# Performance work log

Hardware: AMD Instinct MI355X
Metric: run time of the kernel (lower is better)

## Reference

```python
import jax, jax.numpy as jnp
import numpy as np

C = 64


def setup_inputs() -> dict:
    key = jax.random.key(0)
    ks = jax.random.split(key, 7)
    x = jax.random.normal(ks[0], (8, C, 64, 64), dtype=jnp.float32)
    # 1x1 conv weights stored as [out_c, in_c]; biases [out_c]
    s = 1.0 / np.sqrt(C)
    W1 = jax.random.uniform(ks[1], (C, C), jnp.float32, -s, s)
    b1 = jax.random.uniform(ks[2], (C,), jnp.float32, -s, s)
    W2 = jax.random.uniform(ks[3], (C, C), jnp.float32, -s, s)
    b2 = jax.random.uniform(ks[4], (C,), jnp.float32, -s, s)
    W3 = jax.random.uniform(ks[5], (C, C), jnp.float32, -s, s)
    b3 = jax.random.uniform(ks[6], (C,), jnp.float32, -s, s)
    return {"x": x, "W1": W1, "b1": b1, "W2": W2, "b2": b2, "W3": W3, "b3": b3}


def reference(x, W1, b1, W2, b2, W3, b3):
    gamma = 1.0
    b, c, h, w = x.shape
    xf = x.reshape(b, c, h * w)  # [b, c, n]
    # 1x1 convs == per-pixel channel matmuls
    f = jnp.einsum('oc,bcn->bon', W1, xf) + b1[None, :, None]
    g = jnp.einsum('oc,bcn->bon', W2, xf) + b2[None, :, None]
    k = jnp.einsum('oc,bcn->bon', W3, xf) + b3[None, :, None]
    # scores[b,i,j] = sum_c f[b,c,i] * g[b,c,j]; softmax over j
    scores = jnp.einsum('bci,bcj->bij', f, g)
    attn = jax.nn.softmax(scores, axis=2)
    # out_attn[b,c,i] = sum_j attn[b,i,j] * k[b,c,j]
    out = jnp.einsum('bij,bcj->bci', attn, k).reshape(b, c, h, w)
    return gamma * out + x
```

## Files before the change

kernel.cpp:

```cpp
#include <hip/hip_runtime.h>
#include <hip/hip_bf16.h>

#define NPIX 4096
#define CCH  64
#define NB   8
#define KVBLK 64

typedef __attribute__((ext_vector_type(8)))  short short8;
typedef __attribute__((ext_vector_type(4)))  float f32x4;
typedef __attribute__((ext_vector_type(16))) float f32x16;

#define LOG2E   1.44269504f

__global__ __launch_bounds__(256) void proj_kernel(
    const float* __restrict__ x,
    const float* __restrict__ W1, const float* __restrict__ b1,
    const float* __restrict__ W2, const float* __restrict__ b2,
    const float* __restrict__ W3, const float* __restrict__ b3,
    __hip_bfloat16* __restrict__ Q, __hip_bfloat16* __restrict__ G,
    __hip_bfloat16* __restrict__ K)
{
    const int b  = blockIdx.x >> 6;
    const int i0 = (blockIdx.x & 63) << 6;

    __shared__ float xs[64][65];
    __shared__ float Wt[3][64][68];

    for (int e = threadIdx.x; e < 4096; e += 256) {
        const int c = e >> 6, p = e & 63;
        xs[c][p] = x[(size_t)b * CCH * NPIX + (size_t)c * NPIX + i0 + p];
        Wt[0][e & 63][e >> 6] = W1[e];
        Wt[1][e & 63][e >> 6] = W2[e];
        Wt[2][e & 63][e >> 6] = W3[e];
    }
    __syncthreads();

    const int p = threadIdx.x & 63;
    const int g = threadIdx.x >> 6;

    float acc0[16], acc1[16], acc2[16];
    #pragma unroll
    for (int oo = 0; oo < 16; ++oo) {
        acc0[oo] = b1[g * 16 + oo];
        acc1[oo] = b2[g * 16 + oo];
        acc2[oo] = b3[g * 16 + oo];
    }

    for (int c = 0; c < 64; ++c) {
        const float xv = xs[c][p];
        const f32x4* w0 = (const f32x4*)&Wt[0][c][g * 16];
        const f32x4* w1 = (const f32x4*)&Wt[1][c][g * 16];
        const f32x4* w2 = (const f32x4*)&Wt[2][c][g * 16];
        #pragma unroll
        for (int q = 0; q < 4; ++q) {
            const f32x4 a = w0[q], bb = w1[q], cc = w2[q];
            #pragma unroll
            for (int j = 0; j < 4; ++j) {
                acc0[q * 4 + j] += a[j] * xv;
                acc1[q * 4 + j] += bb[j] * xv;
                acc2[q * 4 + j] += cc[j] * xv;
            }
        }
    }

    const int i = i0 + p;
    #pragma unroll
    for (int oo = 0; oo < 16; ++oo) {
        const int oc = g * 16 + oo;
        Q[(size_t)b * NPIX * CCH + (size_t)i * CCH + oc] = __float2bfloat16(acc0[oo] * LOG2E);
        G[(size_t)b * NPIX * CCH + (size_t)i * CCH + oc] = __float2bfloat16(acc1[oo]);
        K[(size_t)b * CCH * NPIX + (size_t)oc * NPIX + i] = __float2bfloat16(acc2[oo]);
    }
}

__device__ __forceinline__ void gload_lds16(const void* g, void* l) {
    __builtin_amdgcn_global_load_lds(
        (const __attribute__((address_space(1))) unsigned int*)g,
        (__attribute__((address_space(3))) unsigned int*)l, 16, 0, 0);
}
__device__ __forceinline__ unsigned int cvtpk_bf16(float lo, float hi) {
    unsigned int r;
    asm("v_cvt_pk_bf16_f32 %0, %1, %2" : "=v"(r) : "v"(lo), "v"(hi));
    return r;
}
__device__ __forceinline__ float exp2_raw(float x) {
    float r;
    asm("v_exp_f32 %0, %1\n\ts_nop 1" : "=v"(r) : "v"(x));
    return r;
}

__global__ __launch_bounds__(256, 2) void attn_kernel(
    const __hip_bfloat16* __restrict__ Qg, const __hip_bfloat16* __restrict__ Gg,
    const __hip_bfloat16* __restrict__ Kg,
    __hip_bfloat16* __restrict__ Opart, float* __restrict__ Lpart, int split)
{
    __shared__ char lds[2][16384];

    const int blk   = blockIdx.x;
    const int per_b = 16 * split;
    const int b     = blk / per_b;
    const int rem   = blk - b * per_b;
    const int itile = rem / split;
    const int sp    = rem - itile * split;
    const int wave  = threadIdx.x >> 6;
    const int lane  = threadIdx.x & 63;
    const int l32   = lane & 31;
    const int hi    = lane >> 5;
    const int i0w   = itile * 256 + wave * 64;
    const int jcnt  = NPIX / split;
    const int jlo   = sp * jcnt;
    const int niter = jcnt / KVBLK;

    const short* Qb = (const short*)Qg + (size_t)b * NPIX * CCH;
    const char*  Gb = (const char*)(Gg + (size_t)b * NPIX * CCH);
    const char*  Kb = (const char*)(Kg + (size_t)b * CCH * NPIX);

    short8 q[2][4];
    #pragma unroll
    for (int ib = 0; ib < 2; ++ib)
        #pragma unroll
        for (int ks = 0; ks < 4; ++ks)
            q[ib][ks] = *(const short8*)(Qb + (size_t)(i0w + ib * 32 + l32) * CCH + ks * 16 + hi * 8);

    int gbase[2], kbase[2];
    #pragma unroll
    for (int jb = 0; jb < 2; ++jb)
        gbase[jb] = (jb * 32 + l32) * 128 + ((l32 & 7) << 4);
    #pragma unroll
    for (int cb = 0; cb < 2; ++cb)
        kbase[cb] = 8192 + (cb * 32 + l32) * 128 + ((l32 & 7) << 4);

    const char* gsrc[2]; const char* ksrc[2];
    #pragma unroll
    for (int r = 0; r < 2; ++r) {
        const int off = r * 4096 + wave * 1024 + lane * 16;
        const int row = off >> 7, colb = off & 127;
        gsrc[r] = Gb + (size_t)(jlo + row) * 128 + (colb ^ ((row & 7) << 4));
        ksrc[r] = Kb + (size_t)row * 8192 + (size_t)jlo * 2 + (colb ^ ((row & 7) << 4));
    }

    f32x16 zacc;
    #pragma unroll
    for (int r = 0; r < 16; ++r) zacc[r] = 0.f;
    short8 ones;
    #pragma unroll
    for (int t = 0; t < 8; ++t) ones[t] = (short)0x3F80;

    f32x16 o[2][2];
    #pragma unroll
    for (int ib = 0; ib < 2; ++ib)
        #pragma unroll
        for (int cb = 0; cb < 2; ++cb)
            #pragma unroll
            for (int r = 0; r < 16; ++r) o[ib][cb][r] = 0.f;
    f32x16 lacc[2];
    #pragma unroll
    for (int ib = 0; ib < 2; ++ib)
        #pragma unroll
        for (int r = 0; r < 16; ++r) lacc[ib][r] = 0.f;

    auto STAGE = [&](int buf, int tt) {
        #pragma unroll
        for (int r = 0; r < 2; ++r)
            gload_lds16(gsrc[r] + tt * (KVBLK * 128), lds[buf] + r * 4096 + wave * 1024);
        #pragma unroll
        for (int r = 0; r < 2; ++r)
            gload_lds16(ksrc[r] + tt * (KVBLK * 2), lds[buf] + 8192 + r * 4096 + wave * 1024);
    };

    STAGE(0, 0);
    __syncthreads();

    for (int t = 0; t < niter; ++t) {
        const int cur = t & 1;
        STAGE(cur ^ 1, (t + 1 < niter) ? t + 1 : 0);
        const char* L = lds[cur];

        #pragma unroll
        for (int jb = 0; jb < 2; ++jb) {
            short8 ga[4];
            #pragma unroll
            for (int ks = 0; ks < 4; ++ks)
                ga[ks] = *(const short8*)(L + (gbase[jb] ^ ((2 * ks + hi) << 4)));

            short8 pf[2][2];
            #pragma unroll
            for (int ib = 0; ib < 2; ++ib) {
                __builtin_amdgcn_s_setprio(1);
                f32x16 acc = __builtin_amdgcn_mfma_f32_32x32x16_bf16(ga[0], q[ib][0], zacc, 0, 0, 0);
                acc = __builtin_amdgcn_mfma_f32_32x32x16_bf16(ga[1], q[ib][1], acc, 0, 0, 0);
                acc = __builtin_amdgcn_mfma_f32_32x32x16_bf16(ga[2], q[ib][2], acc, 0, 0, 0);
                acc = __builtin_amdgcn_mfma_f32_32x32x16_bf16(ga[3], q[ib][3], acc, 0, 0, 0);
                __builtin_amdgcn_s_setprio(0);
                float p[16];
                #pragma unroll
                for (int r = 0; r < 16; ++r) {
                    const float a = __builtin_amdgcn_fmed3f(acc[r], acc[r], acc[r]);
                    p[r] = exp2_raw(a);
                }
                #pragma unroll
                for (int kk = 0; kk < 2; ++kk) {
                    unsigned int x0 = cvtpk_bf16(p[8 * kk + 0], p[8 * kk + 1]);
                    unsigned int x1 = cvtpk_bf16(p[8 * kk + 2], p[8 * kk + 3]);
                    unsigned int y0 = cvtpk_bf16(p[8 * kk + 4], p[8 * kk + 5]);
                    unsigned int y1 = cvtpk_bf16(p[8 * kk + 6], p[8 * kk + 7]);
                    asm("v_permlane32_swap_b32 %0, %1" : "+v"(x0), "+v"(y0));
                    asm("v_permlane32_swap_b32 %0, %1" : "+v"(x1), "+v"(y1));
                    union { unsigned int u[4]; short8 v; } w;
                    w.u[0] = x0; w.u[1] = x1; w.u[2] = y0; w.u[3] = y1;
                    pf[ib][kk] = w.v;
                }
            }

            __builtin_amdgcn_s_setprio(1);
            #pragma unroll
            for (int kk = 0; kk < 2; ++kk) {
                const int ksg = 2 * jb + kk;
                const short8 ka0 = *(const short8*)(L + (kbase[0] ^ ((2 * ksg + hi) << 4)));
                const short8 ka1 = *(const short8*)(L + (kbase[1] ^ ((2 * ksg + hi) << 4)));
                #pragma unroll
                for (int ib = 0; ib < 2; ++ib) {
                    o[ib][0] = __builtin_amdgcn_mfma_f32_32x32x16_bf16(ka0, pf[ib][kk], o[ib][0], 0, 0, 0);
                    o[ib][1] = __builtin_amdgcn_mfma_f32_32x32x16_bf16(ka1, pf[ib][kk], o[ib][1], 0, 0, 0);
                    lacc[ib] = __builtin_amdgcn_mfma_f32_32x32x16_bf16(ones, pf[ib][kk], lacc[ib], 0, 0, 0);
                }
            }
            __builtin_amdgcn_s_setprio(0);
        }
        __syncthreads();
    }

    const size_t pb = (size_t)(b * split + sp);
    #pragma unroll
    for (int ib = 0; ib < 2; ++ib) {
        #pragma unroll
        for (int cb = 0; cb < 2; ++cb)
            #pragma unroll
            for (int r = 0; r < 16; ++r) {
                const int c = cb * 32 + (r & 3) + 8 * (r >> 2) + 4 * hi;
                const int i = i0w + ib * 32 + l32;
                Opart[(pb * CCH + c) * NPIX + i] = __float2bfloat16(o[ib][cb][r]);
            }
        if (lane < 32)
            Lpart[pb * NPIX + i0w + ib * 32 + l32] = lacc[ib][0];
    }
}

__global__ __launch_bounds__(256) void combine_kernel(
    const __hip_bfloat16* __restrict__ Opart, const float* __restrict__ Lpart,
    const float* __restrict__ x, float* __restrict__ out, int split)
{
    const int b = blockIdx.x >> 6, c = blockIdx.x & 63;
    #pragma unroll
    for (int chunk = 0; chunk < 2; ++chunk) {
        const int i = chunk * 2048 + threadIdx.x * 8;
        float acc[8] = {0,0,0,0,0,0,0,0};
        float Ls[8]  = {0,0,0,0,0,0,0,0};
        for (int s = 0; s < split; ++s) {
            const size_t pb = (size_t)(b * split + s);
            const short8 ov = *(const short8*)((const short*)Opart + (pb * CCH + c) * NPIX + i);
            const f32x4 l0 = *(const f32x4*)&Lpart[pb * NPIX + i];
            const f32x4 l1 = *(const f32x4*)&Lpart[pb * NPIX + i + 4];
            #pragma unroll
            for (int t = 0; t < 8; ++t) {
                union { unsigned int u; float f; } cv;
                cv.u = ((unsigned int)(unsigned short)ov[t]) << 16;
                acc[t] += cv.f;
                Ls[t]  += (t < 4) ? l0[t] : l1[t - 4];
            }
        }
        const size_t idx = ((size_t)b * CCH + c) * NPIX + i;
        const f32x4 xv0 = *(const f32x4*)&x[idx];
        const f32x4 xv1 = *(const f32x4*)&x[idx + 4];
        f32x4 r0, r1;
        #pragma unroll
        for (int t = 0; t < 4; ++t) {
            r0[t] = acc[t] / Ls[t] + xv0[t];
            r1[t] = acc[t + 4] / Ls[t + 4] + xv1[t];
        }
        *(f32x4*)&out[idx]     = r0;
        *(f32x4*)&out[idx + 4] = r1;
    }
}

extern "C" void kernel_launch(void* const* d_in, const int* in_sizes, int n_in,
                              void* d_out, int out_size, void* d_ws, size_t ws_size,
                              hipStream_t stream) {
    const float* x  = (const float*)d_in[0];
    const float* W1 = (const float*)d_in[1];
    const float* b1 = (const float*)d_in[2];
    const float* W2 = (const float*)d_in[3];
    const float* b2 = (const float*)d_in[4];
    const float* W3 = (const float*)d_in[5];
    const float* b3 = (const float*)d_in[6];
    float* out = (float*)d_out;

    char* ws = (char*)d_ws;
    const size_t planeB = (size_t)NB * NPIX * CCH * sizeof(__hip_bfloat16);
    __hip_bfloat16* Q = (__hip_bfloat16*)(ws);
    __hip_bfloat16* G = (__hip_bfloat16*)(ws + planeB);
    __hip_bfloat16* K = (__hip_bfloat16*)(ws + 2 * planeB);

    const size_t base   = 3 * planeB;
    const size_t oPlane = planeB;
    const size_t lPlane = (size_t)NB * NPIX * sizeof(float);

    int split = 8;
    while (split > 1 && base + (size_t)split * (oPlane + lPlane) > ws_size)
        split >>= 1;

    __hip_bfloat16* Opart = (__hip_bfloat16*)(ws + base);
    float* Lpart = (float*)(ws + base + (size_t)split * oPlane);

    proj_kernel<<<dim3(NB * 64), dim3(256), 0, stream>>>(x, W1, b1, W2, b2, W3, b3, Q, G, K);
    attn_kernel<<<dim3(NB * 16 * split), dim3(256), 0, stream>>>(Q, G, K, Opart, Lpart, split);
    combine_kernel<<<dim3(NB * CCH), dim3(256), 0, stream>>>(Opart, Lpart, x, out, split);
}
```

Baseline: 89.19 us.

## Use 8 waves of 32 query rows each and compute row sums in VALU

The attention kernel now runs 512-thread blocks of 8 waves, each owning 32 query rows instead of 64. That halves per-wave accumulator and Q registers and raises the launch-bounds occupancy target. Softmax denominators are now summed on the VALU from the fp32 exponentials with a cross-half shuffle, replacing the extra MFMA against a vector of ones. The G/K staging is redistributed so each thread issues one load per tensor. The trade-off is less K/G data reuse per wave from LDS, and the denominator is summed from fp32 rather than bf16-rounded values.

```diff
diff --git a/kernel.cpp b/kernel.cpp
--- a/kernel.cpp
+++ b/kernel.cpp
@@ -89,7 +89,7 @@
     return r;
 }
 
-__global__ __launch_bounds__(256, 2) void attn_kernel(
+__global__ __launch_bounds__(512, 4) void attn_kernel(
     const __hip_bfloat16* __restrict__ Qg, const __hip_bfloat16* __restrict__ Gg,
     const __hip_bfloat16* __restrict__ Kg,
     __hip_bfloat16* __restrict__ Opart, float* __restrict__ Lpart, int split)
@@ -102,11 +102,12 @@
     const int rem   = blk - b * per_b;
     const int itile = rem / split;
     const int sp    = rem - itile * split;
-    const int wave  = threadIdx.x >> 6;
-    const int lane  = threadIdx.x & 63;
+    const int tid   = threadIdx.x;
+    const int wave  = tid >> 6;
+    const int lane  = tid & 63;
     const int l32   = lane & 31;
     const int hi    = lane >> 5;
-    const int i0w   = itile * 256 + wave * 64;
+    const int i0w   = itile * 256 + wave * 32;
     const int jcnt  = NPIX / split;
     const int jlo   = sp * jcnt;
     const int niter = jcnt / KVBLK;
@@ -115,12 +116,10 @@
     const char*  Gb = (const char*)(Gg + (size_t)b * NPIX * CCH);
     const char*  Kb = (const char*)(Kg + (size_t)b * CCH * NPIX);
 
-    short8 q[2][4];
-    #pragma unroll
-    for (int ib = 0; ib < 2; ++ib)
-        #pragma unroll
-        for (int ks = 0; ks < 4; ++ks)
-            q[ib][ks] = *(const short8*)(Qb + (size_t)(i0w + ib * 32 + l32) * CCH + ks * 16 + hi * 8);
+    short8 q[4];
+    #pragma unroll
+    for (int ks = 0; ks < 4; ++ks)
+        q[ks] = *(const short8*)(Qb + (size_t)(i0w + l32) * CCH + ks * 16 + hi * 8);
 
     int gbase[2], kbase[2];
     #pragma unroll
@@ -130,42 +129,24 @@
     for (int cb = 0; cb < 2; ++cb)
         kbase[cb] = 8192 + (cb * 32 + l32) * 128 + ((l32 & 7) << 4);
 
-    const char* gsrc[2]; const char* ksrc[2];
-    #pragma unroll
-    for (int r = 0; r < 2; ++r) {
-        const int off = r * 4096 + wave * 1024 + lane * 16;
-        const int row = off >> 7, colb = off & 127;
-        gsrc[r] = Gb + (size_t)(jlo + row) * 128 + (colb ^ ((row & 7) << 4));
-        ksrc[r] = Kb + (size_t)row * 8192 + (size_t)jlo * 2 + (colb ^ ((row & 7) << 4));
-    }
+    const int srow = tid >> 3, scolb = (tid & 7) * 16;
+    const char* gsrc = Gb + (size_t)(jlo + srow) * 128 + (scolb ^ ((srow & 7) << 4));
+    const char* ksrc = Kb + (size_t)srow * 8192 + (size_t)jlo * 2 + (scolb ^ ((srow & 7) << 4));
 
     f32x16 zacc;
     #pragma unroll
     for (int r = 0; r < 16; ++r) zacc[r] = 0.f;
-    short8 ones;
-    #pragma unroll
-    for (int t = 0; t < 8; ++t) ones[t] = (short)0x3F80;
-
-    f32x16 o[2][2];
-    #pragma unroll
-    for (int ib = 0; ib < 2; ++ib)
-        #pragma unroll
-        for (int cb = 0; cb < 2; ++cb)
-            #pragma unroll
-            for (int r = 0; r < 16; ++r) o[ib][cb][r] = 0.f;
-    f32x16 lacc[2];
-    #pragma unroll
-    for (int ib = 0; ib < 2; ++ib)
-        #pragma unroll
-        for (int r = 0; r < 16; ++r) lacc[ib][r] = 0.f;
+
+    f32x16 o[2];
+    #pragma unroll
+    for (int cb = 0; cb < 2; ++cb)
+        #pragma unroll
+        for (int r = 0; r < 16; ++r) o[cb][r] = 0.f;
+    float ps = 0.f;
 
     auto STAGE = [&](int buf, int tt) {
-        #pragma unroll
-        for (int r = 0; r < 2; ++r)
-            gload_lds16(gsrc[r] + tt * (KVBLK * 128), lds[buf] + r * 4096 + wave * 1024);
-        #pragma unroll
-        for (int r = 0; r < 2; ++r)
-            gload_lds16(ksrc[r] + tt * (KVBLK * 2), lds[buf] + 8192 + r * 4096 + wave * 1024);
+        gload_lds16(gsrc + tt * (KVBLK * 128), lds[buf] + wave * 1024);
+        gload_lds16(ksrc + tt * (KVBLK * 2),  lds[buf] + 8192 + wave * 1024);
     };
 
     STAGE(0, 0);
@@ -183,33 +164,32 @@
             for (int ks = 0; ks < 4; ++ks)
                 ga[ks] = *(const short8*)(L + (gbase[jb] ^ ((2 * ks + hi) << 4)));
 
-            short8 pf[2][2];
-            #pragma unroll
-            for (int ib = 0; ib < 2; ++ib) {
-                __builtin_amdgcn_s_setprio(1);
-                f32x16 acc = __builtin_amdgcn_mfma_f32_32x32x16_bf16(ga[0], q[ib][0], zacc, 0, 0, 0);
-                acc = __builtin_amdgcn_mfma_f32_32x32x16_bf16(ga[1], q[ib][1], acc, 0, 0, 0);
-                acc = __builtin_amdgcn_mfma_f32_32x32x16_bf16(ga[2], q[ib][2], acc, 0, 0, 0);
-                acc = __builtin_amdgcn_mfma_f32_32x32x16_bf16(ga[3], q[ib][3], acc, 0, 0, 0);
-                __builtin_amdgcn_s_setprio(0);
-                float p[16];
-                #pragma unroll
-                for (int r = 0; r < 16; ++r) {
-                    const float a = __builtin_amdgcn_fmed3f(acc[r], acc[r], acc[r]);
-                    p[r] = exp2_raw(a);
-                }
-                #pragma unroll
-                for (int kk = 0; kk < 2; ++kk) {
-                    unsigned int x0 = cvtpk_bf16(p[8 * kk + 0], p[8 * kk + 1]);
-                    unsigned int x1 = cvtpk_bf16(p[8 * kk + 2], p[8 * kk + 3]);
-                    unsigned int y0 = cvtpk_bf16(p[8 * kk + 4], p[8 * kk + 5]);
-                    unsigned int y1 = cvtpk_bf16(p[8 * kk + 6], p[8 * kk + 7]);
-                    asm("v_permlane32_swap_b32 %0, %1" : "+v"(x0), "+v"(y0));
-                    asm("v_permlane32_swap_b32 %0, %1" : "+v"(x1), "+v"(y1));
-                    union { unsigned int u[4]; short8 v; } w;
-                    w.u[0] = x0; w.u[1] = x1; w.u[2] = y0; w.u[3] = y1;
-                    pf[ib][kk] = w.v;
-                }
+            __builtin_amdgcn_s_setprio(1);
+            f32x16 acc = __builtin_amdgcn_mfma_f32_32x32x16_bf16(ga[0], q[0], zacc, 0, 0, 0);
+            acc = __builtin_amdgcn_mfma_f32_32x32x16_bf16(ga[1], q[1], acc, 0, 0, 0);
+            acc = __builtin_amdgcn_mfma_f32_32x32x16_bf16(ga[2], q[2], acc, 0, 0, 0);
+            acc = __builtin_amdgcn_mfma_f32_32x32x16_bf16(ga[3], q[3], acc, 0, 0, 0);
+            __builtin_amdgcn_s_setprio(0);
+
+            float p[16];
+            #pragma unroll
+            for (int r = 0; r < 16; ++r) {
+                const float a = __builtin_amdgcn_fmed3f(acc[r], acc[r], acc[r]);
+                p[r] = exp2_raw(a);
+                ps += p[r];
+            }
+            short8 pf[2];
+            #pragma unroll
+            for (int kk = 0; kk < 2; ++kk) {
+                unsigned int x0 = cvtpk_bf16(p[8 * kk + 0], p[8 * kk + 1]);
+                unsigned int x1 = cvtpk_bf16(p[8 * kk + 2], p[8 * kk + 3]);
+                unsigned int y0 = cvtpk_bf16(p[8 * kk + 4], p[8 * kk + 5]);
+                unsigned int y1 = cvtpk_bf16(p[8 * kk + 6], p[8 * kk + 7]);
+                asm("v_permlane32_swap_b32 %0, %1" : "+v"(x0), "+v"(y0));
+                asm("v_permlane32_swap_b32 %0, %1" : "+v"(x1), "+v"(y1));
+                union { unsigned int u[4]; short8 v; } w;
+                w.u[0] = x0; w.u[1] = x1; w.u[2] = y0; w.u[3] = y1;
+                pf[kk] = w.v;
             }
 
             __builtin_amdgcn_s_setprio(1);
@@ -218,12 +198,8 @@
                 const int ksg = 2 * jb + kk;
                 const short8 ka0 = *(const short8*)(L + (kbase[0] ^ ((2 * ksg + hi) << 4)));
                 const short8 ka1 = *(const short8*)(L + (kbase[1] ^ ((2 * ksg + hi) << 4)));
-                #pragma unroll
-                for (int ib = 0; ib < 2; ++ib) {
-                    o[ib][0] = __builtin_amdgcn_mfma_f32_32x32x16_bf16(ka0, pf[ib][kk], o[ib][0], 0, 0, 0);
-                    o[ib][1] = __builtin_amdgcn_mfma_f32_32x32x16_bf16(ka1, pf[ib][kk], o[ib][1], 0, 0, 0);
-                    lacc[ib] = __builtin_amdgcn_mfma_f32_32x32x16_bf16(ones, pf[ib][kk], lacc[ib], 0, 0, 0);
-                }
+                o[0] = __builtin_amdgcn_mfma_f32_32x32x16_bf16(ka0, pf[kk], o[0], 0, 0, 0);
+                o[1] = __builtin_amdgcn_mfma_f32_32x32x16_bf16(ka1, pf[kk], o[1], 0, 0, 0);
             }
             __builtin_amdgcn_s_setprio(0);
         }
@@ -232,18 +208,16 @@
 
     const size_t pb = (size_t)(b * split + sp);
     #pragma unroll
-    for (int ib = 0; ib < 2; ++ib) {
-        #pragma unroll
-        for (int cb = 0; cb < 2; ++cb)
-            #pragma unroll
-            for (int r = 0; r < 16; ++r) {
-                const int c = cb * 32 + (r & 3) + 8 * (r >> 2) + 4 * hi;
-                const int i = i0w + ib * 32 + l32;
-                Opart[(pb * CCH + c) * NPIX + i] = __float2bfloat16(o[ib][cb][r]);
-            }
-        if (lane < 32)
-            Lpart[pb * NPIX + i0w + ib * 32 + l32] = lacc[ib][0];
-    }
+    for (int cb = 0; cb < 2; ++cb)
+        #pragma unroll
+        for (int r = 0; r < 16; ++r) {
+            const int c = cb * 32 + (r & 3) + 8 * (r >> 2) + 4 * hi;
+            const int i = i0w + l32;
+            Opart[(pb * CCH + c) * NPIX + i] = __float2bfloat16(o[cb][r]);
+        }
+    ps += __shfl_xor(ps, 32);
+    if (lane < 32)
+        Lpart[pb * NPIX + i0w + l32] = ps;
 }
 
 __global__ __launch_bounds__(256) void combine_kernel(
@@ -313,6 +287,6 @@
     float* Lpart = (float*)(ws + base + (size_t)split * oPlane);
 
     proj_kernel<<<dim3(NB * 64), dim3(256), 0, stream>>>(x, W1, b1, W2, b2, W3, b3, Q, G, K);
-    attn_kernel<<<dim3(NB * 16 * split), dim3(256), 0, stream>>>(Q, G, K, Opart, Lpart, split);
+    attn_kernel<<<dim3(NB * 16 * split), dim3(512), 0, stream>>>(Q, G, K, Opart, Lpart, split);
     combine_kernel<<<dim3(NB * CCH), dim3(256), 0, stream>>>(Opart, Lpart, x, out, split);
 }
```

Result: faster. 86.56 us (-2.9%).
